# Optimization experiments

Hardware: AMD Instinct MI355X
Metric: run time of the kernel (lower is better)

The kernel has to match this reference:

```python
import jax, jax.numpy as jnp
import numpy as np

B, F, S, K = 4, 1024, 2048, 7


def _activate_norm(x):
    # relu -> mean-center over last dim -> L2-normalize scaled by sqrt(n)
    out = jax.nn.relu(x)
    out = out - jnp.mean(out, axis=-1, keepdims=True)
    n = out.shape[-1]
    denom = (jnp.sqrt(jnp.sum(out * out, axis=-1, keepdims=True)) + 1e-5) * (n ** -0.5)
    return out / denom


def _causal_conv(x, w, k):
    # x: [B, C_in, S], w: [C_out, C_in, k]; left-pad by k-1 for causality
    return jax.lax.conv_general_dilated(
        x, w, window_strides=(1,), padding=[(k - 1, 0)],
        dimension_numbers=('NCH', 'OIH', 'NCH'))


def _feed_forward(x, w0, w1, k):
    return _causal_conv(_activate_norm(_causal_conv(x, w0, k)), w1, k)


def setup_inputs() -> dict:
    key = jax.random.key(0)
    ks = jax.random.split(key, 8)
    scale = 0.02
    inp = jax.random.normal(ks[0], (B, F, S), dtype=jnp.float32)
    pos_embd = jax.random.normal(ks[1], (1, F, S), dtype=jnp.float32) * scale
    divisor = jnp.arange(1, F + 1, dtype=jnp.float32).reshape(1, F, 1)
    ws = [jax.random.normal(ks[2 + i], (F, F, K), dtype=jnp.float32) * scale
          for i in range(6)]
    return {
        'inp': inp, 'pos_embd': pos_embd, 'divisor': divisor,
        'depth_w0': ws[0], 'depth_w1': ws[1],
        'point_w0': ws[2], 'point_w1': ws[3],
        'shift_w0': ws[4], 'shift_w1': ws[5],
    }


def reference(inp, pos_embd, divisor, depth_w0, depth_w1, point_w0, point_w1, shift_w0, shift_w1):
    out = inp + pos_embd
    depth = _feed_forward(out, depth_w0, depth_w1, K)
    point = _feed_forward(out, point_w0, point_w1, K)
    shift = _feed_forward(out, shift_w0, shift_w1, K)
    # linear attention: cumsum over feature axis (dim 1), matching depth.cumsum(1)
    return _activate_norm(inp * (jnp.cumsum(depth, axis=1) / divisor + point) + shift)
```

## Files before the change

### kernel.cpp

```cpp
#include <hip/hip_runtime.h>
#include <hip/hip_bf16.h>
#include <stdint.h>

#define B_ 4
#define F_ 1024
#define S_ 2048
#define K_ 7
#define SP_ (S_ + K_ - 1)
#define FC_ 64
#define NC_ (F_ / FC_)
#define FF_ ((size_t)F_ * F_)
#define BFS_ ((size_t)B_ * F_ * S_)
#define BSPF_ ((size_t)B_ * SP_ * F_)

using f32x4 = __attribute__((ext_vector_type(4))) float;
using s16x8 = __attribute__((ext_vector_type(8))) short;
using bf16 = __hip_bfloat16;

typedef const __attribute__((address_space(1))) void gvoid_t;
typedef __attribute__((address_space(3))) void lvoid_t;
__device__ __forceinline__ void async16(const void* g, void* l) {
    __builtin_amdgcn_global_load_lds((gvoid_t*)g, (lvoid_t*)l, 16, 0, 0);
}

__device__ __forceinline__ float bf2f(unsigned short u) {
    union { unsigned int i; float f; } c; c.i = ((unsigned int)u) << 16; return c.f;
}

#define FENCE() asm volatile("" ::: "memory")
#define BARRIER() do { FENCE(); __builtin_amdgcn_s_barrier(); FENCE(); } while (0)

__global__ void zero_pads(bf16* xT, bf16* hT, int nh) {
    int i = blockIdx.x * 256 + threadIdx.x;
    const int per = B_ * (K_ - 1) * F_;
    int total = (1 + nh) * per;
    if (i >= total) return;
    int r = i / per, o = i % per;
    int b = o / ((K_ - 1) * F_);
    int rr = o % ((K_ - 1) * F_);
    bf16 z = __float2bfloat16(0.0f);
    if (r == 0) xT[(size_t)b * SP_ * F_ + rr] = z;
    else        hT[(size_t)(r - 1) * BSPF_ + (size_t)b * SP_ * F_ + rr] = z;
}

__global__ void prep_x(const float* __restrict__ inp, const float* __restrict__ pos,
                       bf16* __restrict__ xT) {
    __shared__ bf16 tile[64][66];
    int b = blockIdx.z;
    int f0 = blockIdx.y * 64, s0 = blockIdx.x * 64;
    int tj = threadIdx.x & 63;
    int t4 = threadIdx.x >> 6;
#pragma unroll
    for (int r = 0; r < 16; ++r) {
        int i = r * 4 + t4;
        size_t off = (size_t)(f0 + i) * S_ + s0 + tj;
        float v = inp[(size_t)b * F_ * S_ + off] + pos[off];
        tile[i][tj] = __float2bfloat16(v);
    }
    __syncthreads();
#pragma unroll
    for (int r = 0; r < 16; ++r) {
        int j = r * 4 + t4;
        xT[(size_t)b * SP_ * F_ + (size_t)(6 + s0 + j) * F_ + f0 + tj] = tile[tj][j];
    }
}

__global__ void wconv(const float* __restrict__ w, bf16* __restrict__ wt) {
    int i = blockIdx.x * 256 + threadIdx.x;
    if (i >= F_ * F_) return;
    const float* src = w + (size_t)i * K_;
#pragma unroll
    for (int t = 0; t < K_; ++t)
        wt[(size_t)t * FF_ + i] = __float2bfloat16(src[t]);
}

__global__ void wconv3(const float* __restrict__ w0, const float* __restrict__ w1,
                       const float* __restrict__ w2, bf16* __restrict__ wt) {
    int i = blockIdx.x * 256 + threadIdx.x;
    int z = blockIdx.y;
    const float* w = (z == 0) ? w0 : (z == 1 ? w1 : w2);
    bf16* dst = wt + (size_t)z * 7 * FF_;
    const float* src = w + (size_t)i * K_;
#pragma unroll
    for (int t = 0; t < K_; ++t)
        dst[(size_t)t * FF_ + i] = __float2bfloat16(src[t]);
}

#define MFMA_QUAD(MB, NB)                                                        \
    __builtin_amdgcn_s_setprio(1);                                               \
    _Pragma("unroll")                                                            \
    for (int kk = 0; kk < 2; ++kk) {                                             \
        _Pragma("unroll")                                                        \
        for (int m = 0; m < 4; ++m) {                                            \
            _Pragma("unroll")                                                    \
            for (int n = 0; n < 2; ++n) {                                        \
                acc[(MB) + m][(NB) + n] = __builtin_amdgcn_mfma_f32_16x16x32_bf16( \
                    af[m][kk], bfr[(NB) + n][kk], acc[(MB) + m][(NB) + n], 0, 0, 0); \
            }                                                                    \
        }                                                                        \
    }                                                                            \
    __builtin_amdgcn_s_setprio(0)

template <bool SPLIT>
__global__ __launch_bounds__(512, 2)
void conv_gemm8(const bf16* __restrict__ Wbase, const bf16* __restrict__ Xbase,
                bf16* __restrict__ O0, bf16* __restrict__ O1,
                long wStride, long xStride, long oStride) {
    __shared__ __align__(16) char lds[147456];

    int wg = blockIdx.x;
    int nchunk = gridDim.x >> 3;
    int swz = (wg & 7) * nchunk + (wg >> 3);
    int kp, r;
    if (SPLIT) { kp = swz & 1; r = swz >> 1; } else { kp = 0; r = swz; }
    int nt = r & 7;
    int mt = (r >> 3) & 3;
    int z  = r >> 5;
    int j = z >> 2, b = z & 3;
    const int kb0 = kp * 8;
    const int kbN = SPLIT ? 8 : 16;
    const int NTp = kbN * 7;

    const bf16* Wbr = Wbase + (size_t)j * wStride;
    const bf16* Xbr = Xbase + (size_t)j * xStride + (size_t)b * SP_ * F_;
    bf16* out = (kp ? O1 : O0) + (size_t)j * oStride + (size_t)b * F_ * S_;
    const int m0 = mt * 256, n0 = nt * 256;

    const int tid = threadIdx.x;
    const int lane = tid & 63, wid = tid >> 6;
    const int wm = wid >> 2, wn = wid & 3;

    const int tid16 = tid * 16;
    const int p0 = tid16, p1 = 8192 + tid16;
    const int lp0 = p0 ^ (((p0 >> 9) & 1) << 5);
    const int lp1 = p1 ^ (((p1 >> 9) & 1) << 5);
    const int stgO0 = (((lp0 >> 11) << 4) + ((lp0 >> 6) & 15)) * F_
                    + (((lp0 >> 10) & 1) << 5) + ((lp0 & 63) >> 1);
    const int stgO1 = (((lp1 >> 11) << 4) + ((lp1 >> 6) & 15)) * F_
                    + (((lp1 >> 10) & 1) << 5) + ((lp1 & 63) >> 1);
    const int bsrc = (((tid16 >> 11) << 4) + ((lp0 >> 6) & 15)) * F_
                   + (((lp0 >> 10) & 1) << 5) + ((lp0 & 63) >> 1);

    const int rA = lane & 15, cA = (lane >> 4) * 8;
    const int swzRC = (rA << 6) + ((cA << 1) ^ (((rA >> 3) & 1) << 5));
    const int aOffBase = wm * 16384 + swzRC;
    int addrB[7];
#pragma unroll
    for (int t = 0; t < 7; ++t) {
        int R = wn * 64 + rA + t;
        addrB[t] = ((R >> 4) << 11) + ((R & 15) << 6)
                 + ((cA << 1) ^ (((R >> 3) & 1) << 5));
    }

    f32x4 acc[8][4] = {};
    s16x8 af[4][2], bfr[4][2];

    auto STGA = [&](int regionByte, const bf16* src) {
        async16(src + stgO0, lds + regionByte + tid16);
        async16(src + stgO1, lds + regionByte + 8192 + tid16);
    };
    auto STGB = [&](int kb1, int pc) {
        const bf16* src = Xbr + (size_t)n0 * F_ + kb1 * 64 + bsrc + pc * 64 * F_;
        async16(src, lds + 65536 + (kb1 & 1) * 40960 + pc * 8192 + tid16);
    };
    auto ASRC = [&](int kb, int t, int h) {
        return Wbr + (size_t)t * FF_ + (size_t)(m0 + h * 128) * F_ + kb * 64;
    };

    STGB(kb0, 0); STGB(kb0, 1); STGB(kb0, 2); STGB(kb0, 3); STGB(kb0, 4);
    STGA(0,     ASRC(kb0, 0, 0));
    STGA(16384, ASRC(kb0, 0, 1));
    STGA(32768, ASRC(kb0, 1, 0));
    asm volatile("s_waitcnt vmcnt(2)" ::: "memory");
    BARRIER();

    for (int kb = kb0; kb < kb0 + kbN; ++kb) {
        const int bB = 65536 + (kb & 1) * 40960;
#pragma unroll
        for (int t = 0; t < 7; ++t) {
            const int ktl = (kb - kb0) * 7 + t;
            const int pA = (kb + t) & 1;
            const char* la = lds + pA * 32768 + aOffBase;
            const char* lb = lds + bB + addrB[t];
            const int t1 = (t == 6) ? 0 : t + 1;
            const int kb1 = (t == 6) ? kb + 1 : kb;
            const int t2 = (t >= 5) ? t - 5 : t + 2;
            const int kb2 = (t >= 5) ? kb + 1 : kb;
            const bool bstage = (t >= 1 && t <= 5) && (kb - kb0) < kbN - 1;

#pragma unroll
            for (int m = 0; m < 4; ++m) {
                af[m][0] = *(const s16x8*)(la + m * 2048);
                af[m][1] = *(const s16x8*)(la + m * 2048 + 1024);
            }
#pragma unroll
            for (int n = 0; n < 2; ++n) {
                bfr[n][0] = *(const s16x8*)(lb + n * 2048);
                bfr[n][1] = *(const s16x8*)(lb + n * 2048 + 1024);
            }
            if (ktl + 1 < NTp) STGA((pA ^ 1) * 32768 + 16384, ASRC(kb1, t1, 1));
            BARRIER();
            MFMA_QUAD(0, 0);
            BARRIER();

#pragma unroll
            for (int n = 0; n < 2; ++n) {
                bfr[2 + n][0] = *(const s16x8*)(lb + (2 + n) * 2048);
                bfr[2 + n][1] = *(const s16x8*)(lb + (2 + n) * 2048 + 1024);
            }
            if (bstage) STGB(kb + 1, t - 1);
            BARRIER();
            MFMA_QUAD(0, 2);
            BARRIER();

#pragma unroll
            for (int m = 0; m < 4; ++m) {
                af[m][0] = *(const s16x8*)(la + (4 + m) * 2048);
                af[m][1] = *(const s16x8*)(la + (4 + m) * 2048 + 1024);
            }
            BARRIER();
            MFMA_QUAD(4, 0);
            BARRIER();

            if (ktl + 2 < NTp) STGA(pA * 32768, ASRC(kb2, t2, 0));
            MFMA_QUAD(4, 2);
            if (ktl < NTp - 2) {
                if (bstage) { asm volatile("s_waitcnt vmcnt(3)" ::: "memory"); }
                else        { asm volatile("s_waitcnt vmcnt(2)" ::: "memory"); }
            } else {
                asm volatile("s_waitcnt vmcnt(0)" ::: "memory");
            }
            BARRIER();
        }
    }

    const int cm = (lane >> 4) * 4, cn = lane & 15;
#pragma unroll
    for (int mf = 0; mf < 8; ++mf)
#pragma unroll
        for (int nf = 0; nf < 4; ++nf)
#pragma unroll
            for (int r2 = 0; r2 < 4; ++r2) {
                int rr = m0 + wm * 128 + mf * 16 + cm + r2;
                int cc = n0 + wn * 64 + nf * 16 + cn;
                out[(size_t)rr * S_ + cc] = __float2bfloat16(acc[mf][nf][r2]);
            }
}

__global__ void addb_stats(const bf16* __restrict__ a, bf16* __restrict__ d,
                           float2* __restrict__ stats) {
    int row = blockIdx.x * 4 + (threadIdx.x >> 6);
    int lane = threadIdx.x & 63;
    const s16x8* pa = (const s16x8*)(a + (size_t)row * S_);
    s16x8* pd = (s16x8*)(d + (size_t)row * S_);
    float s1 = 0.f, s2 = 0.f;
#pragma unroll
    for (int q = 0; q < S_ / 512; ++q) {
        s16x8 va = pa[q * 64 + lane];
        s16x8 vd = pd[q * 64 + lane];
        s16x8 o;
#pragma unroll
        for (int e = 0; e < 8; ++e) {
            float f = bf2f((unsigned short)va[e]) + bf2f((unsigned short)vd[e]);
            bf16 h = __float2bfloat16(f);
            o[e] = (short)__bfloat16_as_ushort(h);
            float rr = fmaxf(__bfloat162float(h), 0.f);
            s1 += rr; s2 += rr * rr;
        }
        pd[q * 64 + lane] = o;
    }
#pragma unroll
    for (int dd = 32; dd; dd >>= 1) { s1 += __shfl_xor(s1, dd); s2 += __shfl_xor(s2, dd); }
    if (lane == 0) {
        float m = s1 / (float)S_;
        float ss = fmaxf(s2 - (float)S_ * m * m, 0.f);
        float denom = (sqrtf(ss) + 1e-5f) * (1.0f / sqrtf((float)S_));
        stats[row] = make_float2(m, 1.0f / denom);
    }
}

__global__ void conv_gemm_small(const bf16* __restrict__ W7, const bf16* __restrict__ xT,
                                bf16* __restrict__ out) {
    __shared__ bf16 tA[128][64];
    __shared__ bf16 tB[128][64];
    int wg = blockIdx.x;
    int cpx = gridDim.x >> 3;
    int swz = (wg & 7) * cpx + (wg >> 3);
    int sx = swz & 15;
    int t1 = swz >> 4;
    int sy = t1 & 7;
    int b = t1 >> 3;
    const bf16* Xbr = xT + (size_t)b * SP_ * F_;
    bf16* ob = out + (size_t)b * F_ * S_;
    int m0 = sy * 128, n0 = sx * 128;
    int tid = threadIdx.x;
    int lane = tid & 63, wid = tid >> 6;
    int wm = wid >> 1, wn = wid & 1;
    f32x4 acc[4][4] = {};
    int srow = tid >> 3, cpart = tid & 7;
    for (int t = 0; t < K_; ++t) {
        const bf16* Wt = W7 + (size_t)t * FF_ + (size_t)m0 * F_;
        const bf16* Xt = Xbr + (size_t)(n0 + t) * F_;
        for (int kb = 0; kb < F_ / 64; ++kb) {
            const bf16* wa = Wt + kb * 64 + cpart * 8;
            const bf16* xa = Xt + kb * 64 + cpart * 8;
#pragma unroll
            for (int q = 0; q < 4; ++q) async16(wa + (size_t)(q * 32 + srow) * F_, &tA[q * 32 + srow][cpart * 8]);
#pragma unroll
            for (int q = 0; q < 4; ++q) async16(xa + (size_t)(q * 32 + srow) * F_, &tB[q * 32 + srow][cpart * 8]);
            __syncthreads();
#pragma unroll
            for (int kk = 0; kk < 2; ++kk) {
                int krow = kk * 32 + (lane >> 4) * 8;
                s16x8 a2[4], b2[4];
#pragma unroll
                for (int m = 0; m < 4; ++m) a2[m] = *(const s16x8*)&tA[wm * 64 + m * 16 + (lane & 15)][krow];
#pragma unroll
                for (int n = 0; n < 4; ++n) b2[n] = *(const s16x8*)&tB[wn * 64 + n * 16 + (lane & 15)][krow];
#pragma unroll
                for (int m = 0; m < 4; ++m)
#pragma unroll
                    for (int n = 0; n < 4; ++n)
                        acc[m][n] = __builtin_amdgcn_mfma_f32_16x16x32_bf16(a2[m], b2[n], acc[m][n], 0, 0, 0);
            }
            __syncthreads();
        }
    }
    int cm = (lane >> 4) * 4, cn = lane & 15;
#pragma unroll
    for (int m = 0; m < 4; ++m)
#pragma unroll
        for (int n = 0; n < 4; ++n)
#pragma unroll
            for (int r = 0; r < 4; ++r)
                ob[(size_t)(m0 + wm * 64 + m * 16 + cm + r) * S_ + n0 + wn * 64 + n * 16 + cn] =
                    __float2bfloat16(acc[m][n][r]);
}

__global__ void rowstats_bf16(const bf16* __restrict__ x, float2* __restrict__ stats) {
    int row = blockIdx.x * 4 + (threadIdx.x >> 6);
    int lane = threadIdx.x & 63;
    const bf16* p = x + (size_t)row * S_;
    float s1 = 0.f, s2 = 0.f;
#pragma unroll
    for (int q = 0; q < S_ / 512; ++q) {
        s16x8 v = *(const s16x8*)(p + q * 512 + lane * 8);
#pragma unroll
        for (int e = 0; e < 8; ++e) {
            float f = fmaxf(bf2f((unsigned short)v[e]), 0.f);
            s1 += f; s2 += f * f;
        }
    }
#pragma unroll
    for (int d = 32; d; d >>= 1) { s1 += __shfl_xor(s1, d); s2 += __shfl_xor(s2, d); }
    if (lane == 0) {
        float m = s1 / (float)S_;
        float ss = fmaxf(s2 - (float)S_ * m * m, 0.f);
        float denom = (sqrtf(ss) + 1e-5f) * (1.0f / sqrtf((float)S_));
        stats[row] = make_float2(m, 1.0f / denom);
    }
}

__global__ void rowstats_f32(const float* __restrict__ x, float2* __restrict__ stats) {
    int row = blockIdx.x * 4 + (threadIdx.x >> 6);
    int lane = threadIdx.x & 63;
    const float* p = x + (size_t)row * S_;
    float s1 = 0.f, s2 = 0.f;
#pragma unroll
    for (int q = 0; q < S_; q += 256) {
        float4 v = *(const float4*)(p + q + lane * 4);
        float a = fmaxf(v.x, 0.f), bb = fmaxf(v.y, 0.f);
        float c = fmaxf(v.z, 0.f), d = fmaxf(v.w, 0.f);
        s1 += a + bb + c + d;
        s2 += a * a + bb * bb + c * c + d * d;
    }
#pragma unroll
    for (int d = 32; d; d >>= 1) { s1 += __shfl_xor(s1, d); s2 += __shfl_xor(s2, d); }
    if (lane == 0) {
        float m = s1 / (float)S_;
        float ss = fmaxf(s2 - (float)S_ * m * m, 0.f);
        float denom = (sqrtf(ss) + 1e-5f) * (1.0f / sqrtf((float)S_));
        stats[row] = make_float2(m, 1.0f / denom);
    }
}

__global__ void normT(const bf16* __restrict__ x, const float2* __restrict__ stats,
                      bf16* __restrict__ hT) {
    __shared__ bf16 tile[64][72];
    int z = blockIdx.z;
    int f0 = blockIdx.y * 64, s0 = blockIdx.x * 64;
    const bf16* xb = x + (size_t)z * F_ * S_;
    bf16* hb = hT + (size_t)z * SP_ * F_;
    const float2* st = stats + (size_t)z * F_;
    int i = threadIdx.x >> 3;
    int c8 = threadIdx.x & 7;
#pragma unroll
    for (int p = 0; p < 2; ++p) {
        int r = i + p * 32;
        float2 s = st[f0 + r];
        s16x8 v = *(const s16x8*)(xb + (size_t)(f0 + r) * S_ + s0 + c8 * 8);
#pragma unroll
        for (int e = 0; e < 8; ++e) {
            float f = fmaxf(bf2f((unsigned short)v[e]), 0.f);
            tile[r][c8 * 8 + e] = __float2bfloat16((f - s.x) * s.y);
        }
    }
    __syncthreads();
    int tj = threadIdx.x & 63;
    int t4 = threadIdx.x >> 6;
#pragma unroll
    for (int r = 0; r < 16; ++r) {
        int jrow = r * 4 + t4;
        hb[(size_t)(6 + s0 + jrow) * F_ + f0 + tj] = tile[tj][jrow];
    }
}

__global__ void combine_partial(const bf16* __restrict__ depth,
                                float* __restrict__ partials) {
    int idx = blockIdx.x * 256 + threadIdx.x;
    int s = idx & (S_ - 1);
    int t = idx / S_;
    int fc = t % NC_;
    int b = t / NC_;
    const bf16* p = depth + (size_t)b * F_ * S_ + (size_t)(fc * FC_) * S_ + s;
    float acc = 0.f;
#pragma unroll
    for (int f = 0; f < FC_; ++f) acc += __bfloat162float(p[(size_t)f * S_]);
    partials[idx] = acc;
}

__global__ void combine_partial2(const bf16* __restrict__ dA, const bf16* __restrict__ dB,
                                 float* __restrict__ partials) {
    int idx = blockIdx.x * 256 + threadIdx.x;
    int s = idx & (S_ - 1);
    int t = idx / S_;
    int fc = t % NC_;
    int b = t / NC_;
    size_t base = (size_t)b * F_ * S_ + (size_t)(fc * FC_) * S_ + s;
    float acc = 0.f;
#pragma unroll
    for (int f = 0; f < FC_; ++f) {
        size_t o = base + (size_t)f * S_;
        acc += __bfloat162float(dA[o]) + __bfloat162float(dB[o]);
    }
    partials[idx] = acc;
}

__global__ void combine_apply(const float* __restrict__ inp, const float* __restrict__ divisor,
                              const bf16* __restrict__ depth, const bf16* __restrict__ point,
                              const bf16* __restrict__ shiftb,
                              const float* __restrict__ partials, float* __restrict__ y) {
    int idx = blockIdx.x * 256 + threadIdx.x;
    int s = idx & (S_ - 1);
    int t = idx / S_;
    int fc = t % NC_;
    int b = t / NC_;
    float acc = 0.f;
    const float* pp = partials + (size_t)b * NC_ * S_ + s;
    for (int c = 0; c < fc; ++c) acc += pp[(size_t)c * S_];
    size_t base = (size_t)b * F_ * S_ + (size_t)(fc * FC_) * S_ + s;
#pragma unroll 4
    for (int f = 0; f < FC_; ++f) {
        size_t o = base + (size_t)f * S_;
        acc += __bfloat162float(depth[o]);
        float yv = inp[o] * (acc / divisor[fc * FC_ + f] + __bfloat162float(point[o]))
                 + __bfloat162float(shiftb[o]);
        y[o] = yv;
    }
}

__global__ void combine_apply2(const float* __restrict__ inp, const float* __restrict__ divisor,
                               const bf16* __restrict__ h0, const bf16* __restrict__ h1,
                               const float* __restrict__ partials, bf16* __restrict__ y) {
    int idx = blockIdx.x * 256 + threadIdx.x;
    int s = idx & (S_ - 1);
    int t = idx / S_;
    int fc = t % NC_;
    int b = t / NC_;
    float acc = 0.f;
    const float* pp = partials + (size_t)b * NC_ * S_ + s;
    for (int c = 0; c < fc; ++c) acc += pp[(size_t)c * S_];
    size_t base = (size_t)b * F_ * S_ + (size_t)(fc * FC_) * S_ + s;
#pragma unroll 4
    for (int f = 0; f < FC_; ++f) {
        size_t o = base + (size_t)f * S_;
        float dep = __bfloat162float(h0[o]) + __bfloat162float(h1[o]);
        float poi = __bfloat162float(h0[o + BFS_]) + __bfloat162float(h1[o + BFS_]);
        float shi = __bfloat162float(h0[o + 2 * BFS_]) + __bfloat162float(h1[o + 2 * BFS_]);
        acc += dep;
        float yv = inp[o] * (acc / divisor[fc * FC_ + f] + poi) + shi;
        y[o] = __float2bfloat16(yv);
    }
}

__global__ void finalnorm(const float* __restrict__ y, const float2* __restrict__ stats,
                          float* __restrict__ out) {
    size_t i = (size_t)blockIdx.x * 256 + threadIdx.x;
    if (i >= (size_t)B_ * F_ * S_) return;
    float2 st = stats[i / S_];
    float v = fmaxf(y[i], 0.f);
    out[i] = (v - st.x) * st.y;
}

__global__ void finalnorm_bf(const bf16* __restrict__ y, const float2* __restrict__ stats,
                             float* __restrict__ out) {
    size_t i8 = (size_t)blockIdx.x * 256 + threadIdx.x;
    size_t row = i8 >> 8;
    float2 st = stats[row];
    s16x8 v = ((const s16x8*)y)[i8];
    float* o = out + i8 * 8;
#pragma unroll
    for (int e = 0; e < 8; ++e) {
        float f = fmaxf(bf2f((unsigned short)v[e]), 0.f);
        o[e] = (f - st.x) * st.y;
    }
}

extern "C" void kernel_launch(void* const* d_in, const int* in_sizes, int n_in,
                              void* d_out, int out_size, void* d_ws, size_t ws_size,
                              hipStream_t stream) {
    const float* inp = (const float*)d_in[0];
    const float* pos = (const float*)d_in[1];
    const float* divisor = (const float*)d_in[2];
    const float* w[6] = { (const float*)d_in[3], (const float*)d_in[4],
                          (const float*)d_in[5], (const float*)d_in[6],
                          (const float*)d_in[7], (const float*)d_in[8] };
    float* out = (float*)d_out;

    size_t off = 0;
    auto alloc = [&](size_t bytes) {
        off = (off + 255) & ~(size_t)255;
        void* r = (char*)d_ws + off;
        off += bytes;
        return r;
    };

    const size_t needB = ((BSPF_ * 2 + 255) & ~255UL)
                       + ((3 * BSPF_ * 2 + 255) & ~255UL)
                       + ((3 * 7 * FF_ * 2 + 255) & ~255UL)
                       + ((3 * BFS_ * 2 + 255) & ~255UL)
                       + ((3 * BFS_ * 2 + 255) & ~255UL)
                       + ((3 * B_ * F_ * 8 + 255) & ~255UL)
                       + ((B_ * NC_ * S_ * 4 + 255) & ~255UL)
                       + 4096;
    const size_t needC = needB + ((3 * BFS_ * 2 + 255) & ~255UL);

    if (ws_size >= needB) {
        const bool splitK = (ws_size >= needC);
        bf16* xT   = (bf16*)alloc(BSPF_ * 2);
        bf16* hT3  = (bf16*)alloc(3 * BSPF_ * 2);
        bf16* Wb3  = (bf16*)alloc(3 * 7 * FF_ * 2);
        bf16* O3   = (bf16*)alloc(3 * BFS_ * 2);
        bf16* br3  = (bf16*)alloc(3 * BFS_ * 2);
        float2* stats3 = (float2*)alloc(3 * B_ * F_ * 8);
        float* partials = (float*)alloc(B_ * NC_ * S_ * 4);
        bf16* P0 = splitK ? (bf16*)alloc(3 * BFS_ * 2) : nullptr;

        zero_pads<<<(4 * B_ * (K_ - 1) * F_ + 255) / 256, 256, 0, stream>>>(xT, hT3, 3);
        prep_x<<<dim3(S_ / 64, F_ / 64, B_), 256, 0, stream>>>(inp, pos, xT);

        wconv3<<<dim3(F_ * F_ / 256, 3), 256, 0, stream>>>(w[0], w[2], w[4], Wb3);
        if (splitK) {
            conv_gemm8<true><<<768, 512, 0, stream>>>(Wb3, xT, P0, O3, 7 * FF_, 0, BFS_);
            addb_stats<<<3 * B_ * F_ / 4, 256, 0, stream>>>(P0, O3, stats3);
        } else {
            conv_gemm8<false><<<384, 512, 0, stream>>>(Wb3, xT, O3, O3, 7 * FF_, 0, BFS_);
            rowstats_bf16<<<3 * B_ * F_ / 4, 256, 0, stream>>>(O3, stats3);
        }
        normT<<<dim3(S_ / 64, F_ / 64, 12), 256, 0, stream>>>(O3, stats3, hT3);

        wconv3<<<dim3(F_ * F_ / 256, 3), 256, 0, stream>>>(w[1], w[3], w[5], Wb3);
        if (splitK) {
            conv_gemm8<true><<<768, 512, 0, stream>>>(Wb3, hT3, P0, br3, 7 * FF_, BSPF_, BFS_);
            bf16* ybf = O3;
            combine_partial2<<<B_ * NC_ * S_ / 256, 256, 0, stream>>>(P0, br3, partials);
            combine_apply2<<<B_ * NC_ * S_ / 256, 256, 0, stream>>>(
                inp, divisor, P0, br3, partials, ybf);
            rowstats_bf16<<<B_ * F_ / 4, 256, 0, stream>>>(ybf, stats3);
            finalnorm_bf<<<(int)(BFS_ / 8 / 256), 256, 0, stream>>>(ybf, stats3, out);
        } else {
            conv_gemm8<false><<<384, 512, 0, stream>>>(Wb3, hT3, br3, br3, 7 * FF_, BSPF_, BFS_);
            float* ybuf = (float*)O3;
            combine_partial<<<B_ * NC_ * S_ / 256, 256, 0, stream>>>(br3, partials);
            combine_apply<<<B_ * NC_ * S_ / 256, 256, 0, stream>>>(
                inp, divisor, br3, br3 + BFS_, br3 + 2 * BFS_, partials, ybuf);
            rowstats_f32<<<B_ * F_ / 4, 256, 0, stream>>>(ybuf, stats3);
            finalnorm<<<(B_ * F_ * S_) / 256, 256, 0, stream>>>(ybuf, stats3, out);
        }
    } else {
        bf16* xT   = (bf16*)alloc(BSPF_ * 2);
        bf16* hT1  = (bf16*)alloc(BSPF_ * 2);
        bf16* Wb1  = (bf16*)alloc(7 * FF_ * 2);
        bf16* O1   = (bf16*)alloc(BFS_ * 2);
        bf16* br3  = (bf16*)alloc(3 * BFS_ * 2);
        float2* stats3 = (float2*)alloc(B_ * F_ * 8);
        float* partials = (float*)alloc(B_ * NC_ * S_ * 4);
        float* ybuf = (float*)xT;

        zero_pads<<<(2 * B_ * (K_ - 1) * F_ + 255) / 256, 256, 0, stream>>>(xT, hT1, 1);
        prep_x<<<dim3(S_ / 64, F_ / 64, B_), 256, 0, stream>>>(inp, pos, xT);

        for (int j = 0; j < 3; ++j) {
            wconv<<<F_ * F_ / 256, 256, 0, stream>>>(w[2 * j], Wb1);
            conv_gemm_small<<<16 * 8 * 4, 256, 0, stream>>>(Wb1, xT, O1);
            rowstats_bf16<<<B_ * F_ / 4, 256, 0, stream>>>(O1, stats3);
            normT<<<dim3(S_ / 64, F_ / 64, 4), 256, 0, stream>>>(O1, stats3, hT1);
            wconv<<<F_ * F_ / 256, 256, 0, stream>>>(w[2 * j + 1], Wb1);
            conv_gemm_small<<<16 * 8 * 4, 256, 0, stream>>>(Wb1, hT1, br3 + j * BFS_);
        }
        combine_partial<<<B_ * NC_ * S_ / 256, 256, 0, stream>>>(br3, partials);
        combine_apply<<<B_ * NC_ * S_ / 256, 256, 0, stream>>>(
            inp, divisor, br3, br3 + BFS_, br3 + 2 * BFS_, partials, ybuf);
        rowstats_f32<<<B_ * F_ / 4, 256, 0, stream>>>(ybuf, stats3);
        finalnorm<<<(B_ * F_ * S_) / 256, 256, 0, stream>>>(ybuf, stats3, out);
    }
}
```

Baseline: 682.3 us.

## Switch conv GEMM inner loop from 16x16x32 to 32x32x16 bf16 MFMA

Replaces the 16x16x32 MFMA tiling in the conv GEMM with 32x32x16 MFMA instructions. Each wave's 128x64 output tile becomes a 4x2 grid of 32x32 accumulators. The LDS fragment addressing, the swizzle XOR handling and the epilogue output indexing are rewritten to match the new register layout. The aim is fewer instructions and LDS reads per FLOP and better fragment reuse. The risks are different register pressure and possible LDS bank conflicts under the new access pattern.

```diff
diff --git a/kernel.cpp b/kernel.cpp
--- a/kernel.cpp
+++ b/kernel.cpp
@@ -14,6 +14,7 @@
 #define BSPF_ ((size_t)B_ * SP_ * F_)
 
 using f32x4 = __attribute__((ext_vector_type(4))) float;
+using f32x16 = __attribute__((ext_vector_type(16))) float;
 using s16x8 = __attribute__((ext_vector_type(8))) short;
 using bf16 = __hip_bfloat16;
 
@@ -86,17 +87,14 @@
         dst[(size_t)t * FF_ + i] = __float2bfloat16(src[t]);
 }
 
-#define MFMA_QUAD(MB, NB)                                                        \
+#define MFMA_OCT(MB, NB)                                                         \
     __builtin_amdgcn_s_setprio(1);                                               \
     _Pragma("unroll")                                                            \
-    for (int kk = 0; kk < 2; ++kk) {                                             \
+    for (int ks = 0; ks < 4; ++ks) {                                             \
         _Pragma("unroll")                                                        \
-        for (int m = 0; m < 4; ++m) {                                            \
-            _Pragma("unroll")                                                    \
-            for (int n = 0; n < 2; ++n) {                                        \
-                acc[(MB) + m][(NB) + n] = __builtin_amdgcn_mfma_f32_16x16x32_bf16( \
-                    af[m][kk], bfr[(NB) + n][kk], acc[(MB) + m][(NB) + n], 0, 0, 0); \
-            }                                                                    \
+        for (int mm = 0; mm < 2; ++mm) {                                         \
+            acc[(MB) + mm][NB] = __builtin_amdgcn_mfma_f32_32x32x16_bf16(        \
+                af[mm][ks], bfr[NB][ks], acc[(MB) + mm][NB], 0, 0, 0);           \
         }                                                                        \
     }                                                                            \
     __builtin_amdgcn_s_setprio(0)
@@ -141,19 +139,27 @@
     const int bsrc = (((tid16 >> 11) << 4) + ((lp0 >> 6) & 15)) * F_
                    + (((lp0 >> 10) & 1) << 5) + ((lp0 & 63) >> 1);
 
-    const int rA = lane & 15, cA = (lane >> 4) * 8;
-    const int swzRC = (rA << 6) + ((cA << 1) ^ (((rA >> 3) & 1) << 5));
-    const int aOffBase = wm * 16384 + swzRC;
-    int addrB[7];
+    const int l31 = lane & 31, l15 = lane & 15, lnH = lane >> 5;
+    const int xorA = ((l31 >> 3) & 1) << 5;
+    const int aBase2 = wm * 16384 + ((l31 >> 4) << 11) + (l15 << 6);
+    int colKsA[4];
+#pragma unroll
+    for (int ks = 0; ks < 4; ++ks)
+        colKsA[ks] = ((ks >> 1) << 10) + ((((ks & 1) << 5) + (lnH << 4)) ^ xorA);
+    int colB0[4];
+#pragma unroll
+    for (int ks = 0; ks < 4; ++ks)
+        colB0[ks] = ((ks >> 1) << 10) + (((ks & 1) << 5) + (lnH << 4));
+    int bRow[7], bXor[7];
 #pragma unroll
     for (int t = 0; t < 7; ++t) {
-        int R = wn * 64 + rA + t;
-        addrB[t] = ((R >> 4) << 11) + ((R & 15) << 6)
-                 + ((cA << 1) ^ (((R >> 3) & 1) << 5));
-    }
-
-    f32x4 acc[8][4] = {};
-    s16x8 af[4][2], bfr[4][2];
+        int R = wn * 64 + l31 + t;
+        bRow[t] = ((R >> 4) << 11) + ((R & 15) << 6);
+        bXor[t] = ((R >> 3) & 1) << 5;
+    }
+
+    f32x16 acc[4][2] = {};
+    s16x8 af[2][4], bfr[2][4];
 
     auto STGA = [&](int regionByte, const bf16* src) {
         async16(src + stgO0, lds + regionByte + tid16);
@@ -180,8 +186,9 @@
         for (int t = 0; t < 7; ++t) {
             const int ktl = (kb - kb0) * 7 + t;
             const int pA = (kb + t) & 1;
-            const char* la = lds + pA * 32768 + aOffBase;
-            const char* lb = lds + bB + addrB[t];
+            const char* la = lds + pA * 32768 + aBase2;
+            const char* lbt = lds + bB + bRow[t];
+            const int bx = bXor[t];
             const int t1 = (t == 6) ? 0 : t + 1;
             const int kb1 = (t == 6) ? kb + 1 : kb;
             const int t2 = (t >= 5) ? t - 5 : t + 2;
@@ -189,41 +196,37 @@
             const bool bstage = (t >= 1 && t <= 5) && (kb - kb0) < kbN - 1;
 
 #pragma unroll
-            for (int m = 0; m < 4; ++m) {
-                af[m][0] = *(const s16x8*)(la + m * 2048);
-                af[m][1] = *(const s16x8*)(la + m * 2048 + 1024);
-            }
-#pragma unroll
-            for (int n = 0; n < 2; ++n) {
-                bfr[n][0] = *(const s16x8*)(lb + n * 2048);
-                bfr[n][1] = *(const s16x8*)(lb + n * 2048 + 1024);
-            }
+            for (int mm = 0; mm < 2; ++mm)
+#pragma unroll
+                for (int ks = 0; ks < 4; ++ks)
+                    af[mm][ks] = *(const s16x8*)(la + mm * 4096 + colKsA[ks]);
+#pragma unroll
+            for (int ks = 0; ks < 4; ++ks)
+                bfr[0][ks] = *(const s16x8*)(lbt + (colB0[ks] ^ bx));
             if (ktl + 1 < NTp) STGA((pA ^ 1) * 32768 + 16384, ASRC(kb1, t1, 1));
             BARRIER();
-            MFMA_QUAD(0, 0);
+            MFMA_OCT(0, 0);
             BARRIER();
 
 #pragma unroll
-            for (int n = 0; n < 2; ++n) {
-                bfr[2 + n][0] = *(const s16x8*)(lb + (2 + n) * 2048);
-                bfr[2 + n][1] = *(const s16x8*)(lb + (2 + n) * 2048 + 1024);
-            }
+            for (int ks = 0; ks < 4; ++ks)
+                bfr[1][ks] = *(const s16x8*)(lbt + 4096 + (colB0[ks] ^ bx));
             if (bstage) STGB(kb + 1, t - 1);
             BARRIER();
-            MFMA_QUAD(0, 2);
+            MFMA_OCT(0, 1);
             BARRIER();
 
 #pragma unroll
-            for (int m = 0; m < 4; ++m) {
-                af[m][0] = *(const s16x8*)(la + (4 + m) * 2048);
-                af[m][1] = *(const s16x8*)(la + (4 + m) * 2048 + 1024);
-            }
+            for (int mm = 0; mm < 2; ++mm)
+#pragma unroll
+                for (int ks = 0; ks < 4; ++ks)
+                    af[mm][ks] = *(const s16x8*)(la + (2 + mm) * 4096 + colKsA[ks]);
             BARRIER();
-            MFMA_QUAD(4, 0);
+            MFMA_OCT(2, 0);
             BARRIER();
 
             if (ktl + 2 < NTp) STGA(pA * 32768, ASRC(kb2, t2, 0));
-            MFMA_QUAD(4, 2);
+            MFMA_OCT(2, 1);
             if (ktl < NTp - 2) {
                 if (bstage) { asm volatile("s_waitcnt vmcnt(3)" ::: "memory"); }
                 else        { asm volatile("s_waitcnt vmcnt(2)" ::: "memory"); }
@@ -234,16 +237,15 @@
         }
     }
 
-    const int cm = (lane >> 4) * 4, cn = lane & 15;
-#pragma unroll
-    for (int mf = 0; mf < 8; ++mf)
-#pragma unroll
-        for (int nf = 0; nf < 4; ++nf)
-#pragma unroll
-            for (int r2 = 0; r2 < 4; ++r2) {
-                int rr = m0 + wm * 128 + mf * 16 + cm + r2;
-                int cc = n0 + wn * 64 + nf * 16 + cn;
-                out[(size_t)rr * S_ + cc] = __float2bfloat16(acc[mf][nf][r2]);
+#pragma unroll
+    for (int mt2 = 0; mt2 < 4; ++mt2)
+#pragma unroll
+        for (int nt2 = 0; nt2 < 2; ++nt2)
+#pragma unroll
+            for (int rg = 0; rg < 16; ++rg) {
+                int rr = m0 + wm * 128 + mt2 * 32 + (rg & 3) + ((rg >> 2) << 3) + (lnH << 2);
+                int cc = n0 + wn * 64 + nt2 * 32 + l31;
+                out[(size_t)rr * S_ + cc] = __float2bfloat16(acc[mt2][nt2][rg]);
             }
 }
 
```

After: 757.3 us. 11.0% more time.
